# Optimization experiments

Hardware: AMD Instinct MI355X
Metric: run time of the kernel (lower is better)

The kernel has to match this reference:

```python
import math
import jax, jax.numpy as jnp
import numpy as np

B, T, D, H, KVH = 2, 2048, 2048, 16, 4
DK = D // H  # 128


def setup_inputs() -> dict:
    key = jax.random.key(0)
    ks = jax.random.split(key, 7)
    q = jax.random.normal(ks[0], (B, T, D), dtype=jnp.float32)
    k = jax.random.normal(ks[1], (B, T, D), dtype=jnp.float32)
    v = jax.random.normal(ks[2], (B, T, D), dtype=jnp.float32)
    # torch Linear weights: (out_features, in_features)
    Wq = jax.random.normal(ks[3], (D, D), dtype=jnp.float32) * 0.02
    Wk = jax.random.normal(ks[4], (KVH * DK, D), dtype=jnp.float32) * 0.02
    Wv = jax.random.normal(ks[5], (KVH * DK, D), dtype=jnp.float32) * 0.02
    Wo = jax.random.normal(ks[6], (D, D), dtype=jnp.float32) * 0.02
    # qk_norm gain, init = log(max_seq_len)
    g = jnp.full((1, H, 1, 1), math.log(2048.0), dtype=jnp.float32)
    return {"q": q, "k": k, "v": v, "Wq": Wq, "Wk": Wk, "Wv": Wv, "Wo": Wo, "g": g}


def _l2norm(x, eps=1e-12):
    # matches torch F.normalize(dim=-1): x / max(||x||, eps)
    n = jnp.sqrt(jnp.sum(x * x, axis=-1, keepdims=True))
    return x / jnp.maximum(n, eps)


def reference(q, k, v, Wq, Wk, Wv, Wo, g):
    b, tq, d = q.shape
    tk = k.shape[1]
    h = g.shape[1]
    dk = d // h
    kvh = Wk.shape[0] // dk

    Q = jnp.einsum('btd,ed->bte', q, Wq).reshape(b, tq, h, dk).transpose(0, 2, 1, 3)     # (B,H,Tq,dk)
    K = jnp.einsum('btd,ed->bte', k, Wk).reshape(b, tk, kvh, dk).transpose(0, 2, 1, 3)   # (B,KVH,Tk,dk)
    V = jnp.einsum('btd,ed->bte', v, Wv).reshape(b, tk, kvh, dk).transpose(0, 2, 1, 3)

    # QK-norm + learned per-head gain
    Q = g * _l2norm(Q)
    K = _l2norm(K)

    # GQA: repeat-interleave kv heads to match query heads (torch enable_gqa)
    rep = h // kvh
    Kr = jnp.repeat(K, rep, axis=1)
    Vr = jnp.repeat(V, rep, axis=1)

    scale = 1.0 / math.sqrt(dk)
    scores = jnp.einsum('bhqd,bhkd->bhqk', Q, Kr) * scale  # (B,H,Tq,Tk)
    causal = jnp.tril(jnp.ones((tq, tk), dtype=bool))
    scores = jnp.where(causal, scores, jnp.finfo(scores.dtype).min)
    A = jax.nn.softmax(scores, axis=-1)
    Y = jnp.einsum('bhqk,bhkd->bhqd', A, Vr)               # (B,H,Tq,dk)
    Y = Y.transpose(0, 2, 1, 3).reshape(b, tq, d)
    return jnp.einsum('btd,ed->bte', Y, Wo)
```

## Files before the change

kernel.cpp:

```cpp
#include <hip/hip_runtime.h>
#include <hip/hip_bf16.h>
#include <stdint.h>

#define B_ 2
#define T_ 2048
#define D_ 2048
#define H_ 16
#define KVH_ 4
#define DK_ 128

typedef __bf16 bf16x8 __attribute__((ext_vector_type(8)));
typedef float f32x4 __attribute__((ext_vector_type(4)));
typedef unsigned short u16x8 __attribute__((ext_vector_type(8)));

typedef __attribute__((address_space(1))) void* gas1_t;
typedef __attribute__((address_space(3))) void* gas3_t;

__device__ __forceinline__ uint16_t f2bf(float f) {
  uint32_t u = __builtin_bit_cast(uint32_t, f);
  u += 0x7FFFu + ((u >> 16) & 1u);
  return (uint16_t)(u >> 16);
}

__device__ __forceinline__ void async16(const void* g, void* l) {
  __builtin_amdgcn_global_load_lds((gas1_t)(uintptr_t)g, (gas3_t)l, 16, 0, 0);
}

__global__ __launch_bounds__(256) void k_cvt_all(const float* __restrict__ q,
                                                 const float* __restrict__ k,
                                                 const float* __restrict__ v,
                                                 const float* __restrict__ wq,
                                                 const float* __restrict__ wk,
                                                 const float* __restrict__ wv,
                                                 const float* __restrict__ wo,
                                                 uint16_t* __restrict__ qb,
                                                 uint16_t* __restrict__ kb,
                                                 uint16_t* __restrict__ vb,
                                                 uint16_t* __restrict__ wqb,
                                                 uint16_t* __restrict__ wkb,
                                                 uint16_t* __restrict__ wvb,
                                                 uint16_t* __restrict__ wob) {
  int gb = blockIdx.x;
  const float* s; uint16_t* d; int base;
  if (gb < 4096)        { s = q;  d = qb;  base = 0; }
  else if (gb < 8192)   { s = k;  d = kb;  base = 4096; }
  else if (gb < 12288)  { s = v;  d = vb;  base = 8192; }
  else if (gb < 14336)  { s = wq; d = wqb; base = 12288; }
  else if (gb < 14848)  { s = wk; d = wkb; base = 14336; }
  else if (gb < 15360)  { s = wv; d = wvb; base = 14848; }
  else                  { s = wo; d = wob; base = 15360; }
  int i = (gb - base) * 256 + threadIdx.x;
  const float4* s4 = (const float4*)s;
  float4 a = s4[(size_t)i * 2], b = s4[(size_t)i * 2 + 1];
  union { uint16_t u[8]; uint4 v; } o;
  o.u[0] = f2bf(a.x); o.u[1] = f2bf(a.y); o.u[2] = f2bf(a.z); o.u[3] = f2bf(a.w);
  o.u[4] = f2bf(b.x); o.u[5] = f2bf(b.y); o.u[6] = f2bf(b.z); o.u[7] = f2bf(b.w);
  ((uint4*)d)[i] = o.v;
}


__global__ __launch_bounds__(256, 2) void k_gemm_bt(const uint16_t* __restrict__ A,
                                                    const uint16_t* __restrict__ Bm,
                                                    float* __restrict__ C,
                                                    int M, int N, int K) {
  __shared__ char smem[49152];
  const int tid = threadIdx.x;
  const int nt = N >> 7;
  const int m0 = (blockIdx.x / nt) << 8;
  const int n0 = (blockIdx.x % nt) << 7;
  const int w = tid >> 6, lane = tid & 63;
  const int wr = (w >> 1) << 6, wc = (w & 1) << 6;
  const int lr = lane & 15;
  const int g16 = ((lane >> 4) << 4);
  const int csw = ((lane & 1) << 6) | (((lane >> 1) & 1) << 5);
  f32x4 acc[8][4] = {};
  const int soff = tid * 16;
  const int scol = ((tid & 7) ^ (((tid >> 3) & 1) << 2) ^ (((tid >> 4) & 1) << 1)) << 3;
  const int srow = tid >> 3;
  const int nk = K >> 6;

  for (int t = 0; t < nk; ++t) {
#pragma unroll
    for (int i = 0; i < 4; ++i) {
      int row = i * 32 + srow;
      async16(A + (size_t)(m0 + row) * K + t * 64 + scol, smem + i * 4096 + soff);
      async16(A + (size_t)(m0 + 128 + row) * K + t * 64 + scol, smem + 16384 + i * 4096 + soff);
      async16(Bm + (size_t)(n0 + row) * K + t * 64 + scol, smem + 32768 + i * 4096 + soff);
    }
    __syncthreads();
#pragma unroll
    for (int kk2 = 0; kk2 < 128; kk2 += 64) {
      bf16x8 aA[4], aB[4], bfr[4];
      const int cb = (kk2 + g16) ^ csw;
#pragma unroll
      for (int m = 0; m < 4; ++m) {
        aA[m] = *(const bf16x8*)(smem + (wr + m * 16 + lr) * 128 + cb);
        aB[m] = *(const bf16x8*)(smem + 16384 + (wr + m * 16 + lr) * 128 + cb);
      }
#pragma unroll
      for (int n = 0; n < 4; ++n)
        bfr[n] = *(const bf16x8*)(smem + 32768 + (wc + n * 16 + lr) * 128 + cb);
#pragma unroll
      for (int m = 0; m < 4; ++m)
#pragma unroll
        for (int n = 0; n < 4; ++n) {
          acc[m][n] = __builtin_amdgcn_mfma_f32_16x16x32_bf16(aA[m], bfr[n], acc[m][n], 0, 0, 0);
          acc[m + 4][n] = __builtin_amdgcn_mfma_f32_16x16x32_bf16(aB[m], bfr[n], acc[m + 4][n], 0, 0, 0);
        }
    }
    __syncthreads();
  }
  const int r0 = (lane >> 4) << 2;
  const int c = lane & 15;
#pragma unroll
  for (int m = 0; m < 8; ++m)
#pragma unroll
    for (int n = 0; n < 4; ++n)
#pragma unroll
      for (int r = 0; r < 4; ++r)
        C[(size_t)(m0 + (m >> 2) * 128 + wr + (m & 3) * 16 + r0 + r) * N +
          n0 + wc + n * 16 + c] = acc[m][n][r];
}

__global__ __launch_bounds__(256, 2) void k_proj(const uint16_t* __restrict__ qb,
                                                 const uint16_t* __restrict__ kb,
                                                 const uint16_t* __restrict__ vb,
                                                 const uint16_t* __restrict__ Wqb,
                                                 const uint16_t* __restrict__ Wkb,
                                                 const uint16_t* __restrict__ Wvb,
                                                 uint16_t* __restrict__ Qn,
                                                 uint16_t* __restrict__ Kn,
                                                 uint16_t* __restrict__ Vt,
                                                 const float* __restrict__ g) {
  __shared__ char smem[49152];
  __shared__ float ssred[2][256];
  const int bid = blockIdx.x;
  int mode, lb;
  if (bid < 64)       { mode = 2; lb = bid; }
  else if (bid < 128) { mode = 1; lb = bid - 64; }
  else                { mode = 0; lb = bid - 128; }
  const uint16_t* A;
  const uint16_t* Bw;
  int nt;
  if (mode == 0)      { A = qb; Bw = Wqb; nt = 16; }
  else if (mode == 1) { A = kb; Bw = Wkb; nt = 4; }
  else                { A = vb; Bw = Wvb; nt = 4; }
  const int m0 = (lb / nt) << 8;
  const int n0 = (lb % nt) << 7;
  const int tid = threadIdx.x;
  const int w = tid >> 6, lane = tid & 63;
  const int wr = (w >> 1) << 6, wc = (w & 1) << 6;
  const int lr = lane & 15;
  const int g16 = ((lane >> 4) << 4);
  const int csw = ((lane & 1) << 6) | (((lane >> 1) & 1) << 5);
  f32x4 acc[8][4] = {};
  const int soff = tid * 16;
  const int scol = ((tid & 7) ^ (((tid >> 3) & 1) << 2) ^ (((tid >> 4) & 1) << 1)) << 3;
  const int srow = tid >> 3;

  for (int t = 0; t < 32; ++t) {
#pragma unroll
    for (int i = 0; i < 4; ++i) {
      int row = i * 32 + srow;
      async16(A + (size_t)(m0 + row) * 2048 + t * 64 + scol, smem + i * 4096 + soff);
      async16(A + (size_t)(m0 + 128 + row) * 2048 + t * 64 + scol, smem + 16384 + i * 4096 + soff);
      async16(Bw + (size_t)(n0 + row) * 2048 + t * 64 + scol, smem + 32768 + i * 4096 + soff);
    }
    __syncthreads();
#pragma unroll
    for (int kk2 = 0; kk2 < 128; kk2 += 64) {
      bf16x8 aA[4], aB[4], bfr[4];
      const int cb = (kk2 + g16) ^ csw;
#pragma unroll
      for (int m = 0; m < 4; ++m) {
        aA[m] = *(const bf16x8*)(smem + (wr + m * 16 + lr) * 128 + cb);
        aB[m] = *(const bf16x8*)(smem + 16384 + (wr + m * 16 + lr) * 128 + cb);
      }
#pragma unroll
      for (int n = 0; n < 4; ++n)
        bfr[n] = *(const bf16x8*)(smem + 32768 + (wc + n * 16 + lr) * 128 + cb);
#pragma unroll
      for (int m = 0; m < 4; ++m)
#pragma unroll
        for (int n = 0; n < 4; ++n) {
          acc[m][n] = __builtin_amdgcn_mfma_f32_16x16x32_bf16(aA[m], bfr[n], acc[m][n], 0, 0, 0);
          acc[m + 4][n] = __builtin_amdgcn_mfma_f32_16x16x32_bf16(aB[m], bfr[n], acc[m + 4][n], 0, 0, 0);
        }
    }
    __syncthreads();
  }

  const int g4 = lane >> 4;
  const int r04 = g4 << 2;
  const int b = m0 >> 11;
  const int t0 = m0 & (T_ - 1);
  const int h = n0 >> 7;

  if (mode <= 1) {
    float ss[8][4];
#pragma unroll
    for (int m = 0; m < 8; ++m)
#pragma unroll
      for (int r = 0; r < 4; ++r) {
        float s = 0.f;
#pragma unroll
        for (int n = 0; n < 4; ++n) s += acc[m][n][r] * acc[m][n][r];
        ss[m][r] = s;
      }
#pragma unroll
    for (int mask = 1; mask < 16; mask <<= 1)
#pragma unroll
      for (int m = 0; m < 8; ++m)
#pragma unroll
        for (int r = 0; r < 4; ++r) ss[m][r] += __shfl_xor(ss[m][r], mask);
#pragma unroll
    for (int m = 0; m < 8; ++m)
#pragma unroll
      for (int r = 0; r < 4; ++r)
        if (lr == (((m & 3) << 2) | r))
          ssred[w & 1][(m >> 2) * 128 + wr + (m & 3) * 16 + g4 * 4 + r] = ss[m][r];
    __syncthreads();
    uint16_t* outp = (mode == 0) ? Qn : Kn;
    const int NHv = (mode == 0) ? H_ : KVH_;
    const float gmul = (mode == 0) ? g[h] * 0.08838834764831845f : 1.0f;
#pragma unroll
    for (int m = 0; m < 8; ++m)
#pragma unroll
      for (int r = 0; r < 4; ++r) {
        int row = (m >> 2) * 128 + wr + (m & 3) * 16 + g4 * 4 + r;
        float tot = ssred[0][row] + ssred[1][row];
        float scl = gmul / fmaxf(sqrtf(tot), 1e-12f);
        size_t base = ((size_t)(b * NHv + h) * T_ + (t0 + row)) * 128;
#pragma unroll
        for (int n = 0; n < 4; ++n)
          outp[base + wc + n * 16 + lr] = f2bf(acc[m][n][r] * scl);
      }
  } else {
    uint16_t* tr = (uint16_t*)smem;
#pragma unroll
    for (int p = 0; p < 2; ++p) {
      __syncthreads();
#pragma unroll
      for (int mm = 0; mm < 4; ++mm)
#pragma unroll
        for (int n = 0; n < 4; ++n)
#pragma unroll
          for (int r = 0; r < 4; ++r)
            tr[(wc + n * 16 + lr) * 132 + (wr + mm * 16 + r04 + r)] = f2bf(acc[p * 4 + mm][n][r]);
      __syncthreads();
      const int qd = tid & 3;
#pragma unroll
      for (int dd = 0; dd < 2; ++dd) {
        int d = (tid >> 2) + dd * 64;
        uint16_t* dst = Vt + ((size_t)(b * KVH_ + h) * 128 + d) * T_ + t0 + p * 128 + qd * 32;
        const uint16_t* srcl = &tr[d * 132 + qd * 32];
#pragma unroll
        for (int j = 0; j < 8; ++j)
          *(ushort4*)(dst + j * 4) = *(const ushort4*)(srcl + j * 4);
      }
    }
  }
}

__global__ __launch_bounds__(256) void k_attn(const uint16_t* __restrict__ Qn,
                                              const uint16_t* __restrict__ Kn,
                                              const uint16_t* __restrict__ Vt,
                                              uint16_t* __restrict__ Y) {
  __shared__ uint16_t Ks[2 * 64 * 128];
  __shared__ uint16_t Vs[2 * 128 * 64];
  __shared__ uint16_t Ps[4 * 16 * 32];
  const int npair = T_ / 128;
  const int pair_id = blockIdx.x % npair;
  const int bh = blockIdx.x / npair;
  const int h = bh % H_;
  const int b = bh / H_;
  const int kvh = h >> 2;
  const int qtA = pair_id;
  const int qtB = (T_ / 64) - 1 - pair_id;
  const uint16_t* Qh = Qn + ((size_t)(b * H_ + h) * T_) * 128;
  const uint16_t* Kh = Kn + ((size_t)(b * KVH_ + kvh) * T_) * 128;
  const uint16_t* Vh = Vt + ((size_t)(b * KVH_ + kvh) * 128) * T_;
  const int tid = threadIdx.x;
  const int w = tid >> 6, lane = tid & 63;
  const int lr = lane & 15;
  const int lk2 = (lane >> 4) << 4;
  const int r0 = (lane >> 4) << 2;
  const int qwA = qtA * 64 + w * 16;
  const int qwB = qtB * 64 + w * 16;
  char* Psw = (char*)Ps + w * 1024;

  bf16x8 qfA[4], qfB[4];
#pragma unroll
  for (int dblk = 0; dblk < 4; ++dblk) {
    qfA[dblk] = *(const bf16x8*)&Qh[(size_t)(qwA + lr) * 128 + dblk * 32 + (lk2 >> 1)];
    qfB[dblk] = *(const bf16x8*)&Qh[(size_t)(qwB + lr) * 128 + dblk * 32 + (lk2 >> 1)];
  }
  union { uint16_t u[8]; bf16x8 v; } ou;
#pragma unroll
  for (int j = 0; j < 8; ++j) ou.u[j] = 0x3F80;
  const bf16x8 ones = ou.v;
  f32x4 oA[8] = {}, oB[8] = {};
  f32x4 sumA = {}, sumB = {};

  auto stageKV = [&](int tile, int buf) {
    const int kv0 = tile * 64;
    char* Kb = (char*)Ks + (buf << 14);
    char* Vb = (char*)Vs + (buf << 14);
#pragma unroll
    for (int i = 0; i < 4; ++i) {
      int off = i * 4096 + tid * 16;
      int krow = off >> 8;
      int kchunk = (off >> 4) & 15;
      int kcol = (kchunk ^ (krow & 7)) << 3;
      async16(Kh + (size_t)(kv0 + krow) * 128 + kcol, Kb + off);
      int vrow = off >> 7;
      int vchunk = (off >> 4) & 7;
      int vcol = (vchunk ^ (vrow & 7)) << 3;
      async16(Vh + (size_t)vrow * T_ + kv0 + vcol, Vb + off);
    }
  };

  auto tilecompute = [&](const bf16x8* qf, f32x4* o, f32x4* sum, int qw, int kv0, int cur) {
    const char* Kb = (const char*)Ks + (cur << 14);
    const char* Vb = (const char*)Vs + (cur << 14);
#pragma unroll
    for (int prr = 0; prr < 2; ++prr) {
#pragma unroll
      for (int kbi = 0; kbi < 2; ++kbi) {
        int kb = prr * 2 + kbi;
        f32x4 s = {};
#pragma unroll
        for (int dblk = 0; dblk < 4; ++dblk) {
          bf16x8 kf = *(const bf16x8*)(Kb +
              ((kb * 16 + lr) << 8) + ((dblk * 64 + lk2) ^ ((lr & 7) << 4)));
          s = __builtin_amdgcn_mfma_f32_16x16x32_bf16(qf[dblk], kf, s, 0, 0, 0);
        }
        int kval = kv0 + kb * 16 + lr;
#pragma unroll
        for (int r = 0; r < 4; ++r) {
          float pv = (kval <= qw + r0 + r) ? __expf(s[r]) : 0.0f;
          *(uint16_t*)(Psw + (r0 + r) * 64 + (((kbi * 16 + lr) * 2) ^ (r << 4))) = f2bf(pv);
        }
      }
      asm volatile("s_waitcnt lgkmcnt(0)" ::: "memory");
      bf16x8 pa = *(const bf16x8*)(Psw + lr * 64 + (lk2 ^ ((lr & 3) << 4)));
#pragma unroll
      for (int dblk = 0; dblk < 8; ++dblk) {
        bf16x8 vf = *(const bf16x8*)(Vb +
            ((dblk * 16 + lr) << 7) + ((prr * 64 + lk2) ^ ((lr & 7) << 4)));
        o[dblk] = __builtin_amdgcn_mfma_f32_16x16x32_bf16(pa, vf, o[dblk], 0, 0, 0);
      }
      *sum = __builtin_amdgcn_mfma_f32_16x16x32_bf16(pa, ones, *sum, 0, 0, 0);
    }
  };

  stageKV(0, 0);
  asm volatile("s_waitcnt vmcnt(0)" ::: "memory");
  __builtin_amdgcn_s_barrier();
  for (int tile = 0; tile <= qtB; ++tile) {
    const int cur = tile & 1;
    if (tile < qtB) stageKV(tile + 1, cur ^ 1);
    const int kv0 = tile * 64;
    tilecompute(qfB, oB, &sumB, qwB, kv0, cur);
    if (tile <= qtA) tilecompute(qfA, oA, &sumA, qwA, kv0, cur);
    asm volatile("s_waitcnt vmcnt(0)" ::: "memory");
    __builtin_amdgcn_s_barrier();
  }

  auto writeout = [&](const f32x4* o, const f32x4& sum, int qw) {
#pragma unroll
    for (int r = 0; r < 4; ++r) {
      float inv = 1.0f / sum[r];
      size_t base = ((size_t)b * T_ + (qw + r0 + r)) * D_ + h * 128 + lr;
#pragma unroll
      for (int dblk = 0; dblk < 8; ++dblk)
        Y[base + dblk * 16] = f2bf(o[dblk][r] * inv);
    }
  };
  writeout(oA, sumA, qwA);
  writeout(oB, sumB, qwB);
}

extern "C" void kernel_launch(void* const* d_in, const int* in_sizes, int n_in,
                              void* d_out, int out_size, void* d_ws, size_t ws_size,
                              hipStream_t stream) {
  (void)in_sizes; (void)n_in; (void)out_size; (void)ws_size;
  const float* q  = (const float*)d_in[0];
  const float* k  = (const float*)d_in[1];
  const float* v  = (const float*)d_in[2];
  const float* Wq = (const float*)d_in[3];
  const float* Wk = (const float*)d_in[4];
  const float* Wv = (const float*)d_in[5];
  const float* Wo = (const float*)d_in[6];
  const float* g  = (const float*)d_in[7];
  float* out = (float*)d_out;
  char* ws = (char*)d_ws;
  const size_t MB = 1ull << 20;
  uint16_t* qb  = (uint16_t*)(ws);
  uint16_t* kb  = (uint16_t*)(ws + 16 * MB);
  uint16_t* vb  = (uint16_t*)(ws + 32 * MB);
  uint16_t* Wqb = (uint16_t*)(ws + 48 * MB);
  uint16_t* Wkb = (uint16_t*)(ws + 56 * MB);
  uint16_t* Wvb = (uint16_t*)(ws + 58 * MB);
  uint16_t* Kn  = (uint16_t*)(ws + 60 * MB);
  uint16_t* Vtb = (uint16_t*)(ws + 64 * MB);
  uint16_t* Wob = (uint16_t*)(ws + 68 * MB);
  uint16_t* Qn  = (uint16_t*)d_out;
  uint16_t* Y   = qb;

  k_cvt_all<<<17408, 256, 0, stream>>>(q, k, v, Wq, Wk, Wv, Wo,
                                       qb, kb, vb, Wqb, Wkb, Wvb, Wob);
  k_proj<<<384, 256, 0, stream>>>(qb, kb, vb, Wqb, Wkb, Wvb, Qn, Kn, Vtb, g);
  k_attn<<<B_ * H_ * (T_ / 128), 256, 0, stream>>>(Qn, Kn, Vtb, Y);
  k_gemm_bt<<<(B_ * T_ / 256) * (D_ / 128), 256, 0, stream>>>(Y, Wob, out, B_ * T_, D_, D_);
}
```

Before: 219.7 us.

## Double-buffer output GEMM with 128x128 tiles and XCD-aware block remapping

The output projection GEMM moves from 256x128 tiles with single-buffered LDS to 128x128 tiles with double-buffered async loads. The next K-slab is prefetched while MFMAs run on the current one, and one barrier per iteration replaces two. Block indices in both the output GEMM and the projection kernel are remapped so that blocks likely to share an XCD work on neighbouring M/N tiles, which should improve L2 reuse. Smaller tiles give twice as many blocks but less register reuse per block.

```diff
diff --git a/kernel.cpp b/kernel.cpp
--- a/kernel.cpp
+++ b/kernel.cpp
@@ -59,67 +59,74 @@
 }
 
 
-__global__ __launch_bounds__(256, 2) void k_gemm_bt(const uint16_t* __restrict__ A,
-                                                    const uint16_t* __restrict__ Bm,
-                                                    float* __restrict__ C,
-                                                    int M, int N, int K) {
-  __shared__ char smem[49152];
+__global__ __launch_bounds__(256) void k_gemm_bt(const uint16_t* __restrict__ A,
+                                                 const uint16_t* __restrict__ Bm,
+                                                 float* __restrict__ C,
+                                                 int M, int N, int K) {
+  __shared__ uint16_t As[2 * 128 * 64];
+  __shared__ uint16_t Bs[2 * 128 * 64];
   const int tid = threadIdx.x;
-  const int nt = N >> 7;
-  const int m0 = (blockIdx.x / nt) << 8;
-  const int n0 = (blockIdx.x % nt) << 7;
+  const int x = blockIdx.x & 7, j = blockIdx.x >> 3;
+  const int m0 = (((x >> 1) << 3) + (j & 7)) << 7;
+  const int n0 = (((x & 1) << 3) + (j >> 3)) << 7;
   const int w = tid >> 6, lane = tid & 63;
   const int wr = (w >> 1) << 6, wc = (w & 1) << 6;
   const int lr = lane & 15;
   const int g16 = ((lane >> 4) << 4);
   const int csw = ((lane & 1) << 6) | (((lane >> 1) & 1) << 5);
-  f32x4 acc[8][4] = {};
+  f32x4 acc[4][4] = {};
   const int soff = tid * 16;
   const int scol = ((tid & 7) ^ (((tid >> 3) & 1) << 2) ^ (((tid >> 4) & 1) << 1)) << 3;
   const int srow = tid >> 3;
   const int nk = K >> 6;
 
-  for (int t = 0; t < nk; ++t) {
+  auto stage = [&](int t, int buf) {
+    char* Ab = (char*)As + (buf << 14);
+    char* Bb = (char*)Bs + (buf << 14);
 #pragma unroll
     for (int i = 0; i < 4; ++i) {
       int row = i * 32 + srow;
-      async16(A + (size_t)(m0 + row) * K + t * 64 + scol, smem + i * 4096 + soff);
-      async16(A + (size_t)(m0 + 128 + row) * K + t * 64 + scol, smem + 16384 + i * 4096 + soff);
-      async16(Bm + (size_t)(n0 + row) * K + t * 64 + scol, smem + 32768 + i * 4096 + soff);
-    }
-    __syncthreads();
+      async16(A + (size_t)(m0 + row) * K + t * 64 + scol, Ab + i * 4096 + soff);
+      async16(Bm + (size_t)(n0 + row) * K + t * 64 + scol, Bb + i * 4096 + soff);
+    }
+  };
+
+  stage(0, 0);
+  asm volatile("s_waitcnt vmcnt(0)" ::: "memory");
+  __builtin_amdgcn_s_barrier();
+  for (int t = 0; t < nk; ++t) {
+    const int cur = t & 1;
+    if (t + 1 < nk) stage(t + 1, cur ^ 1);
+    const char* Ab = (const char*)As + (cur << 14);
+    const char* Bb = (const char*)Bs + (cur << 14);
 #pragma unroll
     for (int kk2 = 0; kk2 < 128; kk2 += 64) {
-      bf16x8 aA[4], aB[4], bfr[4];
+      bf16x8 af[4], bfr[4];
       const int cb = (kk2 + g16) ^ csw;
 #pragma unroll
-      for (int m = 0; m < 4; ++m) {
-        aA[m] = *(const bf16x8*)(smem + (wr + m * 16 + lr) * 128 + cb);
-        aB[m] = *(const bf16x8*)(smem + 16384 + (wr + m * 16 + lr) * 128 + cb);
-      }
+      for (int m = 0; m < 4; ++m)
+        af[m] = *(const bf16x8*)(Ab + (wr + m * 16 + lr) * 128 + cb);
 #pragma unroll
       for (int n = 0; n < 4; ++n)
-        bfr[n] = *(const bf16x8*)(smem + 32768 + (wc + n * 16 + lr) * 128 + cb);
+        bfr[n] = *(const bf16x8*)(Bb + (wc + n * 16 + lr) * 128 + cb);
 #pragma unroll
       for (int m = 0; m < 4; ++m)
 #pragma unroll
-        for (int n = 0; n < 4; ++n) {
-          acc[m][n] = __builtin_amdgcn_mfma_f32_16x16x32_bf16(aA[m], bfr[n], acc[m][n], 0, 0, 0);
-          acc[m + 4][n] = __builtin_amdgcn_mfma_f32_16x16x32_bf16(aB[m], bfr[n], acc[m + 4][n], 0, 0, 0);
-        }
-    }
-    __syncthreads();
+        for (int n = 0; n < 4; ++n)
+          acc[m][n] = __builtin_amdgcn_mfma_f32_16x16x32_bf16(af[m], bfr[n], acc[m][n], 0, 0, 0);
+    }
+    asm volatile("s_waitcnt vmcnt(0)" ::: "memory");
+    __builtin_amdgcn_s_barrier();
   }
   const int r0 = (lane >> 4) << 2;
   const int c = lane & 15;
 #pragma unroll
-  for (int m = 0; m < 8; ++m)
+  for (int m = 0; m < 4; ++m)
 #pragma unroll
     for (int n = 0; n < 4; ++n)
 #pragma unroll
       for (int r = 0; r < 4; ++r)
-        C[(size_t)(m0 + (m >> 2) * 128 + wr + (m & 3) * 16 + r0 + r) * N +
-          n0 + wc + n * 16 + c] = acc[m][n][r];
+        C[(size_t)(m0 + wr + m * 16 + r0 + r) * N + n0 + wc + n * 16 + c] = acc[m][n][r];
 }
 
 __global__ __launch_bounds__(256, 2) void k_proj(const uint16_t* __restrict__ qb,
@@ -141,12 +148,17 @@
   else                { mode = 0; lb = bid - 128; }
   const uint16_t* A;
   const uint16_t* Bw;
-  int nt;
-  if (mode == 0)      { A = qb; Bw = Wqb; nt = 16; }
-  else if (mode == 1) { A = kb; Bw = Wkb; nt = 4; }
-  else                { A = vb; Bw = Wvb; nt = 4; }
-  const int m0 = (lb / nt) << 8;
-  const int n0 = (lb % nt) << 7;
+  if (mode == 0)      { A = qb; Bw = Wqb; }
+  else if (mode == 1) { A = kb; Bw = Wkb; }
+  else                { A = vb; Bw = Wvb; }
+  int mpanel, ntile;
+  {
+    int x = lb & 7, jj = lb >> 3;
+    if (mode == 0) { mpanel = ((x >> 1) << 2) + (jj & 3); ntile = ((x & 1) << 3) + (jj >> 2); }
+    else           { mpanel = (x << 1) + (jj & 1);        ntile = jj >> 1; }
+  }
+  const int m0 = mpanel << 8;
+  const int n0 = ntile << 7;
   const int tid = threadIdx.x;
   const int w = tid >> 6, lane = tid & 63;
   const int wr = (w >> 1) << 6, wc = (w & 1) << 6;
@@ -412,5 +424,5 @@
                                        qb, kb, vb, Wqb, Wkb, Wvb, Wob);
   k_proj<<<384, 256, 0, stream>>>(qb, kb, vb, Wqb, Wkb, Wvb, Qn, Kn, Vtb, g);
   k_attn<<<B_ * H_ * (T_ / 128), 256, 0, stream>>>(Qn, Kn, Vtb, Y);
-  k_gemm_bt<<<(B_ * T_ / 256) * (D_ / 128), 256, 0, stream>>>(Y, Wob, out, B_ * T_, D_, D_);
-}
+  k_gemm_bt<<<(B_ * T_ / 128) * (D_ / 128), 256, 0, stream>>>(Y, Wob, out, B_ * T_, D_, D_);
+}
```

Result: faster. 197.8 us (-10.0%).
